# Performance work log

Hardware: AMD Instinct MI355X
Metric: run time of the kernel (lower is better)

## Reference

```python
import jax, jax.numpy as jnp
import numpy as np

NUM_HEADS = 16


def rotate_half(x):
    half = x.shape[-1] // 2
    return jnp.concatenate((-x[..., half:], x[..., :half]), axis=-1)


def rope_tables(seq_len, head_dim, dtype=jnp.float32):
    inv_freq = 1.0 / (10000.0 ** (jnp.arange(0, head_dim, 2, dtype=jnp.float32) / head_dim))
    t = jnp.arange(seq_len, dtype=jnp.float32)
    freqs = jnp.outer(t, inv_freq)                 # [S, hd/2]
    emb = jnp.concatenate((freqs, freqs), axis=-1)  # [S, hd]
    return jnp.cos(emb).astype(dtype), jnp.sin(emb).astype(dtype)


def setup_inputs() -> dict:
    key = jax.random.key(0)
    k1, k2, k3 = jax.random.split(key, 3)
    B, S, D = 2, 2048, 1024
    x = jax.random.normal(k1, (B, S, D), dtype=jnp.float32)
    # causal lower-triangular mask, broadcast over batch/heads
    mask = jnp.tril(jnp.ones((S, S), dtype=bool))[None, None, :, :]
    w_qkv = jax.random.normal(k2, (3 * D, D), dtype=jnp.float32) * (D ** -0.5)
    w_out = jax.random.normal(k3, (D, D), dtype=jnp.float32) * (D ** -0.5)
    return {"x": x, "mask": mask, "w_qkv": w_qkv, "w_out": w_out}


def reference(x, mask, w_qkv, w_out):
    B, S, D = x.shape
    H = NUM_HEADS
    hd = D // H
    scale = hd ** -0.5

    qkv = jnp.einsum('bsd,ed->bse', x, w_qkv)          # [B, S, 3D]
    q, k, v = jnp.split(qkv, 3, axis=-1)

    def split(t):
        return t.reshape(B, S, H, hd).transpose(0, 2, 1, 3)  # [B, H, S, hd]

    q, k, v = split(q), split(k), split(v)

    cos, sin = rope_tables(S, hd, x.dtype)             # [S, hd]
    cos = cos[None, None]
    sin = sin[None, None]
    q = q * cos + rotate_half(q) * sin
    k = k * cos + rotate_half(k) * sin

    attn = jnp.einsum('bhqd,bhkd->bhqk', q, k) * scale  # [B, H, S, S]
    attn = jnp.where(mask, attn, jnp.float32(-jnp.inf).astype(attn.dtype))
    attn = jax.nn.softmax(attn, axis=-1)
    out = jnp.einsum('bhqk,bhkd->bhqd', attn, v)        # [B, H, S, hd]
    out = out.transpose(0, 2, 1, 3).reshape(B, S, D)
    return jnp.einsum('bsd,ed->bse', out, w_out)
```

## Files before the change

### kernel.cpp

```cpp
#include <hip/hip_runtime.h>
#include <hip/hip_bf16.h>

typedef __attribute__((ext_vector_type(8))) __bf16 bf16x8;
typedef __attribute__((ext_vector_type(4))) __bf16 bf16x4;
typedef __attribute__((ext_vector_type(2))) __bf16 bf16x2;
typedef __attribute__((ext_vector_type(4))) float f32x4;
typedef __attribute__((ext_vector_type(16))) float f32x16;

#define SEQ 2048
#define NH 16
#define HD 64
#define DMODEL 1024
#define BATCH 2
#define MTOT 4096
#define NSLOT 72

#if __has_builtin(__builtin_amdgcn_exp2f)
#define EXP2(x) __builtin_amdgcn_exp2f(x)
#else
#define EXP2(x) exp2f(x)
#endif
#define MFMA32(a, b, c) __builtin_amdgcn_mfma_f32_32x32x16_bf16(a, b, c, 0, 0, 0)

__device__ __forceinline__ void gl_lds16(const void* g, void* l) {
    __builtin_amdgcn_global_load_lds(
        (const __attribute__((address_space(1))) void*)(uintptr_t)g,
        (__attribute__((address_space(3))) void*)(uintptr_t)l,
        16, 0, 0);
}

__device__ __forceinline__ unsigned pk2(float x, float y) {
    union { bf16x2 h; unsigned u; } c;
    c.h = bf16x2{ (__bf16)x, (__bf16)y };
    return c.u;
}

__constant__ int4 FITEM[80] = {
    {31,0,16,68},{31,16,32,69},{31,32,48,70},{31,48,64,71},
    {23,0,16,37},{23,16,32,38},{23,32,48,39},
    {15,0,16,14},{15,16,32,15},
    {30,15,31,65},{30,46,62,67},
    {22,30,46,36},
    {7,0,16,-1},
    {29,0,15,60},{29,15,30,61},{29,30,45,62},{29,45,60,63},
    {30,0,15,64},{30,31,46,66},
    {22,0,15,34},{22,15,30,35},
    {21,14,29,32},{21,29,44,33},
    {28,14,29,57},{28,43,58,59},
    {14,0,15,12},{14,15,30,13},
    {27,0,14,52},{27,14,28,53},{27,28,42,54},{27,42,56,55},
    {28,0,14,56},{28,29,43,58},
    {20,0,14,28},{20,14,28,29},{20,28,42,30},
    {21,0,14,31},
    {26,13,27,49},{26,40,54,51},
    {19,26,40,27},
    {13,0,14,10},{13,14,28,11},
    {6,0,14,-1},
    {25,0,13,44},{25,13,26,45},{25,26,39,46},{25,39,52,47},
    {26,0,13,48},{26,27,40,50},
    {24,12,25,41},{24,37,50,43},
    {19,0,13,25},{19,13,26,26},
    {18,12,25,23},{18,25,38,24},
    {12,0,13,8},{12,13,26,9},
    {24,0,12,40},{24,25,37,42},
    {17,0,12,19},{17,12,24,20},{17,24,36,21},
    {18,0,12,22},
    {16,22,34,18},
    {11,0,12,6},{11,12,24,7},
    {5,0,12,-1},
    {16,0,11,16},{16,11,22,17},
    {10,0,11,4},{10,11,22,5},
    {9,0,10,2},{9,10,20,3},
    {4,0,10,-1},
    {8,0,9,0},{8,9,18,1},
    {3,0,8,-1},{2,0,6,-1},{1,0,4,-1},{0,0,2,-1}
};

__global__ __launch_bounds__(256) void cast3(const float4* __restrict__ x,
                                             const float4* __restrict__ wq,
                                             const float4* __restrict__ wo,
                                             __bf16* __restrict__ xb,
                                             __bf16* __restrict__ wqb,
                                             __bf16* __restrict__ wob) {
    const int NX  = 1024 * 1024;
    const int NWQ = 768 * 1024;
    const int NTOT = NX + NWQ + 256 * 1024;
    int i = blockIdx.x * 256 + threadIdx.x;
    if (i >= NTOT) return;
    float4 v; __bf16* dst; int j;
    if (i < NX)            { j = i;            v = x[j];  dst = xb;  }
    else if (i < NX + NWQ) { j = i - NX;       v = wq[j]; dst = wqb; }
    else                   { j = i - NX - NWQ; v = wo[j]; dst = wob; }
    bf16x4 o = { (__bf16)v.x, (__bf16)v.y, (__bf16)v.z, (__bf16)v.w };
    *(bf16x4*)(dst + (size_t)j * 4) = o;
}

__global__ __launch_bounds__(256) void gemm_qkv(const __bf16* __restrict__ A,
                                                const __bf16* __restrict__ Bt,
                                                __bf16* __restrict__ Qp,
                                                char* __restrict__ K2,
                                                char* __restrict__ V2) {
    const int K = 1024;
    __shared__ __bf16 sA[2][128 * 64];
    __shared__ __bf16 sB[2][128 * 64];
    const int tid = threadIdx.x, lane = tid & 63, wave = tid >> 6;
    const int lrow = lane & 15, quad = lane >> 4;

    int lin = blockIdx.y * 24 + blockIdx.x;
    lin = (lin & 7) * 96 + (lin >> 3);
    const int bx = lin % 24, by = lin / 24;
    const int m0 = by * 128, n0 = bx * 128;
    const int wm = wave >> 1, wn = wave & 1;

    const __bf16* ap[4]; const __bf16* bp[4]; int ldso[4];
#pragma unroll
    for (int i = 0; i < 4; ++i) {
        int r0 = i * 32 + wave * 8;
        int row = r0 + (lane >> 3);
        int cg = (lane & 7) ^ (row & 7);
        ap[i] = A + (size_t)(m0 + row) * K + cg * 8;
        bp[i] = Bt + (size_t)(n0 + row) * K + cg * 8;
        ldso[i] = r0 * 128;
    }
    int arow[4], brow[4];
#pragma unroll
    for (int i = 0; i < 4; ++i) {
        arow[i] = wm * 64 + i * 16 + lrow;
        brow[i] = wn * 64 + i * 16 + lrow;
    }

    f32x4 z = {0.f, 0.f, 0.f, 0.f};
    f32x4 acc[4][4];
#pragma unroll
    for (int i = 0; i < 4; ++i)
#pragma unroll
        for (int j = 0; j < 4; ++j) acc[i][j] = z;

    char* sA0 = (char*)sA[0]; char* sA1 = (char*)sA[1];
    char* sB0 = (char*)sB[0]; char* sB1 = (char*)sB[1];

    auto STAGE = [&](char* dA, char* dB, int k0) {
#pragma unroll
        for (int i = 0; i < 4; ++i) gl_lds16(ap[i] + k0, dA + ldso[i]);
#pragma unroll
        for (int i = 0; i < 4; ++i) gl_lds16(bp[i] + k0, dB + ldso[i]);
    };
    auto COMPUTE = [&](const char* sAb, const char* sBb) {
#pragma unroll
        for (int ks = 0; ks < 2; ++ks) {
            bf16x8 af[4], bfr[4];
#pragma unroll
            for (int i = 0; i < 4; ++i)
                af[i] = *(const bf16x8*)(sAb + arow[i] * 128 +
                                         (((ks * 4 + quad) ^ (arow[i] & 7)) << 4));
#pragma unroll
            for (int i = 0; i < 4; ++i)
                bfr[i] = *(const bf16x8*)(sBb + brow[i] * 128 +
                                          (((ks * 4 + quad) ^ (brow[i] & 7)) << 4));
#pragma unroll
            for (int i = 0; i < 4; ++i)
#pragma unroll
                for (int j = 0; j < 4; ++j)
                    acc[i][j] = __builtin_amdgcn_mfma_f32_16x16x32_bf16(
                        af[i], bfr[j], acc[i][j], 0, 0, 0);
        }
    };

    STAGE(sA0, sB0, 0);
    __syncthreads();
    for (int k0 = 0; k0 < K; k0 += 128) {
        if (k0 + 64 < K) STAGE(sA1, sB1, k0 + 64);
        COMPUTE(sA0, sB0);
        __syncthreads();
        if (k0 + 128 < K) STAGE(sA0, sB0, k0 + 128);
        COMPUTE(sA1, sB1);
        __syncthreads();
    }

    const int nt = bx;
    const int sec = nt >> 3;
    const int b = m0 >> 11;
    const int s0b = m0 & (SEQ - 1);
    const int h = (nt & 7) * 2 + wn;
    const int bh = b * NH + h;

    if (sec < 2) {
        const float scale = sec ? 1.0f : 0.18033688011112042f;
        char* Kb = K2 + (size_t)bh * 262144;
        float invf0 = 0.15915494309189535f *
                      exp2f(-(float)lrow * 0.4152410118609203f);
        float invf1 = invf0 * 0.01f;
#pragma unroll
        for (int i = 0; i < 4; ++i) {
            int srow0 = s0b + wm * 64 + i * 16 + quad * 4;
#pragma unroll
            for (int j = 0; j < 2; ++j) {
                float invf = j ? invf1 : invf0;
                int hdlo = j * 16 + lrow;
#pragma unroll
                for (int r = 0; r < 4; ++r) {
                    int s = srow0 + r;
                    float rev = (float)s * invf;
                    float fr = rev - floorf(rev);
                    float sn = __builtin_amdgcn_sinf(fr);
                    float cs = __builtin_amdgcn_cosf(fr);
                    float lo = acc[i][j][r], hi = acc[i][j + 2][r];
                    float olo = (lo * cs - hi * sn) * scale;
                    float ohi = (hi * cs + lo * sn) * scale;
                    if (sec == 0) {
                        size_t base = ((size_t)bh * SEQ + s) * HD + hdlo;
                        Qp[base] = (__bf16)olo;
                        Qp[base + 32] = (__bf16)ohi;
                    } else {
                        char* kt = Kb + (s >> 5) * 4096 + (s & 31) * 16 +
                                   ((lrow >> 3) & 1) * 512 + (lrow & 7) * 2;
                        *(__bf16*)(kt + j * 1024) = (__bf16)olo;
                        *(__bf16*)(kt + (j + 2) * 1024) = (__bf16)ohi;
                    }
                }
            }
        }
    } else {
        char* Vb = V2 + (size_t)bh * 262144;
#pragma unroll
        for (int i = 0; i < 4; ++i) {
            int srow0 = s0b + wm * 64 + i * 16 + quad * 4;
            int kb = srow0 >> 4, ko = srow0 & 15;
            int slot0 = ((ko >> 2) & 1) * 8 + (ko >> 3) * 4;
#pragma unroll
            for (int j = 0; j < 4; ++j) {
                int ch = j * 16 + lrow;
                bf16x4 wv = { (__bf16)acc[i][j][0], (__bf16)acc[i][j][1],
                              (__bf16)acc[i][j][2], (__bf16)acc[i][j][3] };
                *(bf16x4*)(Vb + kb * 2048 + ch * 32 + slot0 * 2) = wv;
            }
        }
    }
}

__global__ __launch_bounds__(256) void gemm_bt(const __bf16* __restrict__ A,
                                               const __bf16* __restrict__ Bt,
                                               float* __restrict__ Cf,
                                               int M, int N, int K) {
    __shared__ __bf16 sA[2][128 * 64];
    __shared__ __bf16 sB[2][128 * 64];
    const int tid = threadIdx.x, lane = tid & 63, wave = tid >> 6;
    const int lrow = lane & 15, quad = lane >> 4;

    int lin = blockIdx.y * 8 + blockIdx.x;
    lin = (lin & 7) * 32 + (lin >> 3);
    const int bx = lin & 7, by = lin >> 3;
    const int m0 = by * 128, n0 = bx * 128;
    const int wm = wave >> 1, wn = wave & 1;

    const __bf16* ap[4]; const __bf16* bp[4]; int ldso[4];
#pragma unroll
    for (int i = 0; i < 4; ++i) {
        int r0 = i * 32 + wave * 8;
        int row = r0 + (lane >> 3);
        int cg = (lane & 7) ^ (row & 7);
        ap[i] = A + (size_t)(m0 + row) * K + cg * 8;
        bp[i] = Bt + (size_t)(n0 + row) * K + cg * 8;
        ldso[i] = r0 * 128;
    }
    int arow[4], brow[4];
#pragma unroll
    for (int i = 0; i < 4; ++i) {
        arow[i] = wm * 64 + i * 16 + lrow;
        brow[i] = wn * 64 + i * 16 + lrow;
    }

    f32x4 z = {0.f, 0.f, 0.f, 0.f};
    f32x4 acc[4][4];
#pragma unroll
    for (int i = 0; i < 4; ++i)
#pragma unroll
        for (int j = 0; j < 4; ++j) acc[i][j] = z;

    char* sA0 = (char*)sA[0]; char* sA1 = (char*)sA[1];
    char* sB0 = (char*)sB[0]; char* sB1 = (char*)sB[1];

    auto STAGE = [&](char* dA, char* dB, int k0) {
#pragma unroll
        for (int i = 0; i < 4; ++i) gl_lds16(ap[i] + k0, dA + ldso[i]);
#pragma unroll
        for (int i = 0; i < 4; ++i) gl_lds16(bp[i] + k0, dB + ldso[i]);
    };
    auto COMPUTE = [&](const char* sAb, const char* sBb) {
#pragma unroll
        for (int ks = 0; ks < 2; ++ks) {
            bf16x8 af[4], bfr[4];
#pragma unroll
            for (int i = 0; i < 4; ++i)
                af[i] = *(const bf16x8*)(sAb + arow[i] * 128 +
                                         (((ks * 4 + quad) ^ (arow[i] & 7)) << 4));
#pragma unroll
            for (int i = 0; i < 4; ++i)
                bfr[i] = *(const bf16x8*)(sBb + brow[i] * 128 +
                                          (((ks * 4 + quad) ^ (brow[i] & 7)) << 4));
#pragma unroll
            for (int i = 0; i < 4; ++i)
#pragma unroll
                for (int j = 0; j < 4; ++j)
                    acc[i][j] = __builtin_amdgcn_mfma_f32_16x16x32_bf16(
                        af[i], bfr[j], acc[i][j], 0, 0, 0);
        }
    };

    STAGE(sA0, sB0, 0);
    __syncthreads();
    for (int k0 = 0; k0 < K; k0 += 128) {
        if (k0 + 64 < K) STAGE(sA1, sB1, k0 + 64);
        COMPUTE(sA0, sB0);
        __syncthreads();
        if (k0 + 128 < K) STAGE(sA0, sB0, k0 + 128);
        COMPUTE(sA1, sB1);
        __syncthreads();
    }
#pragma unroll
    for (int i = 0; i < 4; ++i)
#pragma unroll
        for (int j = 0; j < 4; ++j)
#pragma unroll
            for (int r = 0; r < 4; ++r) {
                int row = m0 + wm * 64 + i * 16 + quad * 4 + r;
                int col = n0 + wn * 64 + j * 16 + lrow;
                Cf[(size_t)row * N + col] = acc[i][j][r];
            }
}

__global__ __launch_bounds__(64) void flash_attn(const __bf16* __restrict__ Qp,
                                                 const char* __restrict__ K2,
                                                 const char* __restrict__ V2,
                                                 __bf16* __restrict__ Aout,
                                                 __bf16* __restrict__ Opart,
                                                 float* __restrict__ Lpart) {
    const int lane = threadIdx.x;
    const int ql = lane & 31, half = lane >> 5;
    const int bh = blockIdx.x;
    const int4 it = FITEM[blockIdx.y];
    const int s = it.x, t0 = it.y, t1 = it.z, slot = it.w;
    const int b = bh >> 4, hh = bh & 15;

    const __bf16* qb = Qp + ((size_t)bh * SEQ + s * 64 + ql) * HD + half * 8;
    bf16x8 qf0[4], qf1[4];
#pragma unroll
    for (int kc = 0; kc < 4; ++kc) {
        qf0[kc] = *(const bf16x8*)(qb + kc * 16);
        qf1[kc] = *(const bf16x8*)(qb + 32 * HD + kc * 16);
    }
    const char* Kb = K2 + (size_t)bh * 262144 + half * 512 + ql * 16;
    const char* Vb = V2 + (size_t)bh * 262144 + ql * 32 + half * 16;

    f32x16 zz = {0.f};
    f32x16 oA0 = zz, oA1 = zz, oB0 = zz, oB1 = zz;
    float lA = 0.f, lB = 0.f;
    const int dA = 2 * s, dB = 2 * s + 1;
    const int thr = ql - 4 * half;

    auto STEP = [&](int t, const bf16x8* kf, bf16x8* kn) {
        bf16x8 vf[2][2];
#pragma unroll
        for (int lo = 0; lo < 2; ++lo) {
            const char* vp = Vb + (t * 2 + lo) * 2048;
            vf[lo][0] = *(const bf16x8*)(vp);
            vf[lo][1] = *(const bf16x8*)(vp + 1024);
        }
        if (t + 1 < t1) {
            const char* kt = Kb + (t + 1) * 4096;
#pragma unroll
            for (int kc = 0; kc < 4; ++kc)
                kn[kc] = *(const bf16x8*)(kt + kc * 1024);
        }
        const bool do0 = (t != dB);
        f32x16 st0 = zz, st1 = zz;
        if (do0) {
#pragma unroll
            for (int kc = 0; kc < 4; ++kc)
                st0 = MFMA32(kf[kc], qf0[kc], st0);
        }
#pragma unroll
        for (int kc = 0; kc < 4; ++kc)
            st1 = MFMA32(kf[kc], qf1[kc], st1);

        if (do0) {
#pragma unroll
            for (int i = 0; i < 16; ++i) st0[i] = EXP2(st0[i]);
            if (t == dA) {
#pragma unroll
                for (int g = 0; g < 4; ++g)
#pragma unroll
                    for (int tt = 0; tt < 4; ++tt)
                        if (8 * g + tt > thr) st0[g * 4 + tt] = 0.f;
            }
#pragma unroll
            for (int i = 0; i < 16; ++i) lA += st0[i];
        }
#pragma unroll
        for (int i = 0; i < 16; ++i) st1[i] = EXP2(st1[i]);
        if (t == dB) {
#pragma unroll
            for (int g = 0; g < 4; ++g)
#pragma unroll
                for (int tt = 0; tt < 4; ++tt)
                    if (8 * g + tt > thr) st1[g * 4 + tt] = 0.f;
        }
#pragma unroll
        for (int i = 0; i < 16; ++i) lB += st1[i];

#pragma unroll
        for (int lo = 0; lo < 2; ++lo) {
            if (do0) {
                union { unsigned u[4]; bf16x8 v; } p0;
#pragma unroll
                for (int d = 0; d < 4; ++d)
                    p0.u[d] = pk2(st0[lo * 8 + 2 * d], st0[lo * 8 + 2 * d + 1]);
                oA0 = MFMA32(vf[lo][0], p0.v, oA0);
                oA1 = MFMA32(vf[lo][1], p0.v, oA1);
            }
            union { unsigned u[4]; bf16x8 v; } p1;
#pragma unroll
            for (int d = 0; d < 4; ++d)
                p1.u[d] = pk2(st1[lo * 8 + 2 * d], st1[lo * 8 + 2 * d + 1]);
            oB0 = MFMA32(vf[lo][0], p1.v, oB0);
            oB1 = MFMA32(vf[lo][1], p1.v, oB1);
        }
    };

    bf16x8 kA[4], kB[4];
    {
        const char* kt = Kb + t0 * 4096;
#pragma unroll
        for (int kc = 0; kc < 4; ++kc)
            kA[kc] = *(const bf16x8*)(kt + kc * 1024);
    }
    int t = t0;
    while (true) {
        STEP(t, kA, kB);
        if (++t >= t1) break;
        STEP(t, kB, kA);
        if (++t >= t1) break;
    }

    lA += __shfl_xor(lA, 32, 64);
    lB += __shfl_xor(lB, 32, 64);

    if (slot < 0) {
        float iA = 1.0f / lA, iB = 1.0f / lB;
        __bf16* oa = Aout + ((size_t)b * SEQ + s * 64 + ql) * DMODEL + hh * HD;
        __bf16* ob = oa + (size_t)32 * DMODEL;
#pragma unroll
        for (int g = 0; g < 4; ++g) {
            bf16x4 wA0 = { (__bf16)(oA0[g*4+0]*iA), (__bf16)(oA0[g*4+1]*iA),
                           (__bf16)(oA0[g*4+2]*iA), (__bf16)(oA0[g*4+3]*iA) };
            bf16x4 wA1 = { (__bf16)(oA1[g*4+0]*iA), (__bf16)(oA1[g*4+1]*iA),
                           (__bf16)(oA1[g*4+2]*iA), (__bf16)(oA1[g*4+3]*iA) };
            bf16x4 wB0 = { (__bf16)(oB0[g*4+0]*iB), (__bf16)(oB0[g*4+1]*iB),
                           (__bf16)(oB0[g*4+2]*iB), (__bf16)(oB0[g*4+3]*iB) };
            bf16x4 wB1 = { (__bf16)(oB1[g*4+0]*iB), (__bf16)(oB1[g*4+1]*iB),
                           (__bf16)(oB1[g*4+2]*iB), (__bf16)(oB1[g*4+3]*iB) };
            *(bf16x4*)(oa + 8 * g + 4 * half) = wA0;
            *(bf16x4*)(oa + 32 + 8 * g + 4 * half) = wA1;
            *(bf16x4*)(ob + 8 * g + 4 * half) = wB0;
            *(bf16x4*)(ob + 32 + 8 * g + 4 * half) = wB1;
        }
    } else {
        __bf16* oa = Opart + ((size_t)(bh * NSLOT + slot) << 12) + ql * 64;
        __bf16* ob = oa + 32 * 64;
#pragma unroll
        for (int g = 0; g < 4; ++g) {
            bf16x4 wA0 = { (__bf16)oA0[g*4+0], (__bf16)oA0[g*4+1],
                           (__bf16)oA0[g*4+2], (__bf16)oA0[g*4+3] };
            bf16x4 wA1 = { (__bf16)oA1[g*4+0], (__bf16)oA1[g*4+1],
                           (__bf16)oA1[g*4+2], (__bf16)oA1[g*4+3] };
            bf16x4 wB0 = { (__bf16)oB0[g*4+0], (__bf16)oB0[g*4+1],
                           (__bf16)oB0[g*4+2], (__bf16)oB0[g*4+3] };
            bf16x4 wB1 = { (__bf16)oB1[g*4+0], (__bf16)oB1[g*4+1],
                           (__bf16)oB1[g*4+2], (__bf16)oB1[g*4+3] };
            *(bf16x4*)(oa + 8 * g + 4 * half) = wA0;
            *(bf16x4*)(oa + 32 + 8 * g + 4 * half) = wA1;
            *(bf16x4*)(ob + 8 * g + 4 * half) = wB0;
            *(bf16x4*)(ob + 32 + 8 * g + 4 * half) = wB1;
        }
        if (!half) {
            Lpart[(bh * NSLOT + slot) * 64 + ql] = lA;
            Lpart[(bh * NSLOT + slot) * 64 + 32 + ql] = lB;
        }
    }
}

__global__ __launch_bounds__(256) void combine(const __bf16* __restrict__ Opart,
                                               const float* __restrict__ Lpart,
                                               __bf16* __restrict__ Aout) {
    const int bh = blockIdx.x;
    const int s = 8 + blockIdx.y;
    const int C = (s < 16) ? 2 : ((s < 24) ? 3 : 4);
    const int base = (s < 16) ? (s - 8) * 2
                   : (s < 24) ? 16 + (s - 16) * 3
                              : 40 + (s - 24) * 4;
    const int t = threadIdx.x;
    const int r = t >> 2, cg = (t & 3) * 16;
    float acc[16];
#pragma unroll
    for (int i = 0; i < 16; ++i) acc[i] = 0.f;
    float l = 0.f;
    for (int ci = 0; ci < C; ++ci) {
        int ch = bh * NSLOT + base + ci;
        l += Lpart[ch * 64 + r];
        const __bf16* p = Opart + ((size_t)ch << 12) + r * 64 + cg;
#pragma unroll
        for (int k = 0; k < 2; ++k) {
            bf16x8 v = ((const bf16x8*)p)[k];
#pragma unroll
            for (int j = 0; j < 8; ++j) acc[k * 8 + j] += (float)v[j];
        }
    }
    float invl = 1.0f / l;
    const int b = bh >> 4, hh = bh & 15;
    __bf16* dst = Aout + ((size_t)(b * SEQ + s * 64 + r)) * DMODEL +
                  hh * 64 + cg;
#pragma unroll
    for (int k = 0; k < 2; ++k) {
        bf16x8 w;
#pragma unroll
        for (int j = 0; j < 8; ++j) w[j] = (__bf16)(acc[k * 8 + j] * invl);
        ((bf16x8*)dst)[k] = w;
    }
}

extern "C" void kernel_launch(void* const* d_in, const int* in_sizes, int n_in,
                              void* d_out, int out_size, void* d_ws, size_t ws_size,
                              hipStream_t stream) {
    (void)in_sizes; (void)n_in; (void)out_size; (void)ws_size;
    const float* x  = (const float*)d_in[0];
    const float* wq = (const float*)d_in[2];
    const float* wo = (const float*)d_in[3];
    float* out = (float*)d_out;

    char* w = (char*)d_ws;
    __bf16* xb   = (__bf16*)(w);
    __bf16* wqb  = (__bf16*)(w + (8ull << 20));
    __bf16* wob  = (__bf16*)(w + (14ull << 20));
    __bf16* Opart= (__bf16*)(w + (16ull << 20));
    float*  Lpart= (float*) (w + (35ull << 20));
    __bf16* Qb   = (__bf16*)(w + (40ull << 20));
    char*   K2   = (char*)  (w + (48ull << 20));
    char*   V2   = (char*)  (w + (56ull << 20));
    __bf16* aob  = xb;

    cast3<<<8192, 256, 0, stream>>>((const float4*)x, (const float4*)wq,
                                    (const float4*)wo, xb, wqb, wob);
    gemm_qkv<<<dim3(24, 32), 256, 0, stream>>>(xb, wqb, Qb, K2, V2);
    flash_attn<<<dim3(32, 80), 64, 0, stream>>>(Qb, K2, V2, aob, Opart, Lpart);
    combine<<<dim3(32, 24), 256, 0, stream>>>(Opart, Lpart, aob);
    gemm_bt<<<dim3(8, 32), 256, 0, stream>>>(aob, wob, out, MTOT, 1024, 1024);
}
```

Measured before the change: 185.4 us.

## Triple-buffer QKV GEMM with 256x128 tiles, 8 waves and vmcnt-based sync

Reworks the QKV projection GEMM to use a 256x128 block tile with 512 threads. It keeps a three-stage LDS ring filled by direct global-to-LDS loads, and waits with a partial vmcnt before each barrier so that two tiles stay in flight. MFMA sections are wrapped in raised wave priority, and the block-index swizzle is dropped. The goal is to hide global load latency and reuse each B tile across more rows. The cost is a large LDS footprint (about 147 KB), which limits occupancy to one block per CU, and half as many blocks, which may leave a tail on the last wave of blocks.

Result: no change. 184.7 us (-0.4%).

```diff
diff --git a/kernel.cpp b/kernel.cpp
--- a/kernel.cpp
+++ b/kernel.cpp
@@ -34,6 +34,12 @@
     c.h = bf16x2{ (__bf16)x, (__bf16)y };
     return c.u;
 }
+
+#define TILE_SYNC(N) do {                                           \
+    asm volatile("s_waitcnt vmcnt(" #N ")" ::: "memory");           \
+    __builtin_amdgcn_s_barrier();                                   \
+    __builtin_amdgcn_sched_barrier(0);                              \
+} while (0)
 
 __constant__ int4 FITEM[80] = {
     {31,0,16,68},{31,16,32,69},{31,32,48,70},{31,48,64,71},
@@ -95,32 +101,36 @@
     *(bf16x4*)(dst + (size_t)j * 4) = o;
 }
 
-__global__ __launch_bounds__(256) void gemm_qkv(const __bf16* __restrict__ A,
-                                                const __bf16* __restrict__ Bt,
-                                                __bf16* __restrict__ Qp,
-                                                char* __restrict__ K2,
-                                                char* __restrict__ V2) {
+__global__ __launch_bounds__(512, 2) void gemm_qkv(const __bf16* __restrict__ A,
+                                                   const __bf16* __restrict__ Bt,
+                                                   __bf16* __restrict__ Qp,
+                                                   char* __restrict__ K2,
+                                                   char* __restrict__ V2) {
     const int K = 1024;
-    __shared__ __bf16 sA[2][128 * 64];
-    __shared__ __bf16 sB[2][128 * 64];
+    __shared__ __align__(16) char lds[3 * 49152];
     const int tid = threadIdx.x, lane = tid & 63, wave = tid >> 6;
     const int lrow = lane & 15, quad = lane >> 4;
-
-    int lin = blockIdx.y * 24 + blockIdx.x;
-    lin = (lin & 7) * 96 + (lin >> 3);
-    const int bx = lin % 24, by = lin / 24;
-    const int m0 = by * 128, n0 = bx * 128;
+    const int bx = blockIdx.x, by = blockIdx.y;
+    const int m0 = by * 256, n0 = bx * 128;
     const int wm = wave >> 1, wn = wave & 1;
 
-    const __bf16* ap[4]; const __bf16* bp[4]; int ldso[4];
+    const __bf16* ap[4]; int aof[4];
+    const __bf16* bp[2]; int bof[2];
 #pragma unroll
     for (int i = 0; i < 4; ++i) {
-        int r0 = i * 32 + wave * 8;
+        int r0 = i * 64 + wave * 8;
         int row = r0 + (lane >> 3);
         int cg = (lane & 7) ^ (row & 7);
         ap[i] = A + (size_t)(m0 + row) * K + cg * 8;
+        aof[i] = r0 * 128;
+    }
+#pragma unroll
+    for (int i = 0; i < 2; ++i) {
+        int r0 = i * 64 + wave * 8;
+        int row = r0 + (lane >> 3);
+        int cg = (lane & 7) ^ (row & 7);
         bp[i] = Bt + (size_t)(n0 + row) * K + cg * 8;
-        ldso[i] = r0 * 128;
+        bof[i] = 32768 + r0 * 128;
     }
     int arow[4], brow[4];
 #pragma unroll
@@ -136,46 +146,47 @@
 #pragma unroll
         for (int j = 0; j < 4; ++j) acc[i][j] = z;
 
-    char* sA0 = (char*)sA[0]; char* sA1 = (char*)sA[1];
-    char* sB0 = (char*)sB[0]; char* sB1 = (char*)sB[1];
-
-    auto STAGE = [&](char* dA, char* dB, int k0) {
-#pragma unroll
-        for (int i = 0; i < 4; ++i) gl_lds16(ap[i] + k0, dA + ldso[i]);
-#pragma unroll
-        for (int i = 0; i < 4; ++i) gl_lds16(bp[i] + k0, dB + ldso[i]);
+    auto STAGE = [&](char* base, int k0) {
+#pragma unroll
+        for (int i = 0; i < 4; ++i) gl_lds16(ap[i] + k0, base + aof[i]);
+#pragma unroll
+        for (int i = 0; i < 2; ++i) gl_lds16(bp[i] + k0, base + bof[i]);
     };
-    auto COMPUTE = [&](const char* sAb, const char* sBb) {
+    auto COMPUTE = [&](const char* base) {
+        const char* bb = base + 32768;
 #pragma unroll
         for (int ks = 0; ks < 2; ++ks) {
             bf16x8 af[4], bfr[4];
 #pragma unroll
             for (int i = 0; i < 4; ++i)
-                af[i] = *(const bf16x8*)(sAb + arow[i] * 128 +
+                af[i] = *(const bf16x8*)(base + arow[i] * 128 +
                                          (((ks * 4 + quad) ^ (arow[i] & 7)) << 4));
 #pragma unroll
             for (int i = 0; i < 4; ++i)
-                bfr[i] = *(const bf16x8*)(sBb + brow[i] * 128 +
+                bfr[i] = *(const bf16x8*)(bb + brow[i] * 128 +
                                           (((ks * 4 + quad) ^ (brow[i] & 7)) << 4));
+            __builtin_amdgcn_s_setprio(1);
 #pragma unroll
             for (int i = 0; i < 4; ++i)
 #pragma unroll
                 for (int j = 0; j < 4; ++j)
                     acc[i][j] = __builtin_amdgcn_mfma_f32_16x16x32_bf16(
                         af[i], bfr[j], acc[i][j], 0, 0, 0);
+            __builtin_amdgcn_s_setprio(0);
         }
     };
 
-    STAGE(sA0, sB0, 0);
-    __syncthreads();
-    for (int k0 = 0; k0 < K; k0 += 128) {
-        if (k0 + 64 < K) STAGE(sA1, sB1, k0 + 64);
-        COMPUTE(sA0, sB0);
-        __syncthreads();
-        if (k0 + 128 < K) STAGE(sA0, sB0, k0 + 128);
-        COMPUTE(sA1, sB1);
-        __syncthreads();
-    }
+    STAGE(lds, 0);
+    STAGE(lds + 49152, 64);
+    TILE_SYNC(6);
+    for (int t = 0; t < 14; ++t) {
+        STAGE(lds + ((t + 2) % 3) * 49152, (t + 2) * 64);
+        COMPUTE(lds + (t % 3) * 49152);
+        TILE_SYNC(6);
+    }
+    COMPUTE(lds + 2 * 49152);
+    TILE_SYNC(0);
+    COMPUTE(lds);
 
     const int nt = bx;
     const int sec = nt >> 3;
@@ -550,7 +561,7 @@
 
     cast3<<<8192, 256, 0, stream>>>((const float4*)x, (const float4*)wq,
                                     (const float4*)wo, xb, wqb, wob);
-    gemm_qkv<<<dim3(24, 32), 256, 0, stream>>>(xb, wqb, Qb, K2, V2);
+    gemm_qkv<<<dim3(24, 16), 512, 0, stream>>>(xb, wqb, Qb, K2, V2);
     flash_attn<<<dim3(32, 80), 64, 0, stream>>>(Qb, K2, V2, aob, Opart, Lpart);
     combine<<<dim3(32, 24), 256, 0, stream>>>(Opart, Lpart, aob);
     gemm_bt<<<dim3(8, 32), 256, 0, stream>>>(aob, wob, out, MTOT, 1024, 1024);
```
